# Kernel optimization log

Measured on AMD Instinct MI355X. Metric: run time of the kernel, lower is better.

Reference implementation:

```python
import jax, jax.numpy as jnp
import numpy as np

NUM_BITS_ACTS = 8
NUM_BITS_PARAMS = 8
NUM_BITS_ACCUM = 32


def quantized_range(num_bits):
    # distiller-style signed range: [-2^(n-1), 2^(n-1)-1]
    n = 2.0 ** num_bits
    return -n / 2.0, n / 2.0 - 1.0


def sym_scale(num_bits, sat_abs):
    # scale = (2^(n-1)-1) / max_abs
    return (2.0 ** (num_bits - 1) - 1.0) / sat_abs


def quant_clamp(t, scale, qmin, qmax):
    return jnp.clip(jnp.round(t * scale), qmin, qmax)


def setup_inputs() -> dict:
    key = jax.random.key(0)
    kx, kw = jax.random.split(key)
    x = jax.random.normal(kx, (8192, 4096), dtype=jnp.float32)
    W = jax.random.normal(kw, (4096, 4096), dtype=jnp.float32)  # [out, in]
    return {"x": x, "W": W}


def reference(x, W):
    acts_min, acts_max = quantized_range(NUM_BITS_ACTS)
    params_min, params_max = quantized_range(NUM_BITS_PARAMS)
    accum_min, accum_max = quantized_range(NUM_BITS_ACCUM)

    # __init__: quantize weights once (symmetric, max-abs)
    w_scale = sym_scale(NUM_BITS_PARAMS, jnp.max(jnp.abs(W)))
    W_q = quant_clamp(W, w_scale, params_min, params_max)

    # pre_quantized_forward: input scale from max-abs, quantize-clamp input
    in_scale = sym_scale(NUM_BITS_ACTS, jnp.max(jnp.abs(x)))
    x_q = quant_clamp(x, in_scale, acts_min, acts_max)

    # wrapped Linear in integer domain, clamp to accumulator range
    accum = jnp.clip(x_q @ W_q.T, accum_min, accum_max)  # [8192, 4096]

    # post_quantized_forward: requantize accumulator to output range
    accum_scale = in_scale * w_scale
    accum_max_abs = jnp.max(jnp.abs(accum))
    y_f_max_abs = accum_max_abs / accum_scale
    out_scale = sym_scale(NUM_BITS_ACTS, y_f_max_abs)
    requant_scale = out_scale / accum_scale

    out_q = quant_clamp(accum, requant_scale, acts_min, acts_max)
    out_f = out_q / out_scale  # dequantize
    return out_f
```

## Files before the change

### kernel.cpp

```cpp
#include <hip/hip_runtime.h>
#include <stdint.h>


using i32x4 = __attribute__((ext_vector_type(4))) int;

#define M_DIM 8192
#define N_DIM 4096
#define K_DIM 4096

#define BM 256
#define BN 256
#define BKB 128
#define NKT (K_DIM / BKB)

__global__ void k_init(unsigned* sc) {
    sc[0] = 0u;
    sc[1] = 0u;
    sc[2] = 0u;
}

__global__ __launch_bounds__(256) void k_absmax2(const float4* __restrict__ x,
                                                 const float4* __restrict__ w,
                                                 unsigned* __restrict__ sc) {
    const bool isX = blockIdx.x < 2048;
    const float4* src = isX ? x : w;
    const int n4 = isX ? (M_DIM * K_DIM / 4) : (N_DIM * K_DIM / 4);
    const int brel = isX ? blockIdx.x : (blockIdx.x - 2048);
    const int nb = isX ? 2048 : 1024;
    unsigned m = 0;
    for (int i = brel * 256 + threadIdx.x; i < n4; i += nb * 256) {
        float4 v = src[i];
        unsigned a = __float_as_uint(v.x) & 0x7fffffffu;
        unsigned b = __float_as_uint(v.y) & 0x7fffffffu;
        unsigned c = __float_as_uint(v.z) & 0x7fffffffu;
        unsigned d = __float_as_uint(v.w) & 0x7fffffffu;
        m = max(m, max(max(a, b), max(c, d)));
    }
    for (int off = 32; off; off >>= 1)
        m = max(m, (unsigned)__shfl_xor((int)m, off));
    __shared__ unsigned wm[4];
    int ln = threadIdx.x & 63, wv = threadIdx.x >> 6;
    if (ln == 0) wm[wv] = m;
    __syncthreads();
    if (threadIdx.x == 0)
        atomicMax(sc + (isX ? 0 : 1), max(max(wm[0], wm[1]), max(wm[2], wm[3])));
}

__global__ __launch_bounds__(256) void k_quant2(const float4* __restrict__ x,
                                                const float4* __restrict__ w,
                                                unsigned* __restrict__ xq,
                                                unsigned* __restrict__ wq,
                                                const unsigned* __restrict__ sc) {
    const bool isX = blockIdx.x < 2048;
    const float4* src = isX ? x : w;
    unsigned* dst = isX ? xq : wq;
    const int n4 = isX ? (M_DIM * K_DIM / 4) : (N_DIM * K_DIM / 4);
    const int brel = isX ? blockIdx.x : (blockIdx.x - 2048);
    const int nb = isX ? 2048 : 1024;
    const float scale = 127.0f / __uint_as_float(sc[isX ? 0 : 1]);
    for (int i = brel * 256 + threadIdx.x; i < n4; i += nb * 256) {
        float4 v = src[i];
        int q0 = min(127, max(-128, (int)rintf(v.x * scale)));
        int q1 = min(127, max(-128, (int)rintf(v.y * scale)));
        int q2 = min(127, max(-128, (int)rintf(v.z * scale)));
        int q3 = min(127, max(-128, (int)rintf(v.w * scale)));
        dst[i] = (unsigned)(q0 & 0xff) | ((unsigned)(q1 & 0xff) << 8) |
                 ((unsigned)(q2 & 0xff) << 16) | ((unsigned)(q3 & 0xff) << 24);
    }
}

__global__ __launch_bounds__(512, 2) void k_gemm(const char* __restrict__ Aq,
                                                 const char* __restrict__ Bq,
                                                 int* __restrict__ C,
                                                 unsigned* __restrict__ maxAcc) {
    __shared__ __align__(16) char lds[131072];
    __shared__ int wmax[8];

    const int t = threadIdx.x;
    const int ln = t & 63;
    const int wv = t >> 6;
    const int wr = wv >> 2;
    const int wc = wv & 3;
    const int lr = ln & 15;
    const int lk = ln >> 4;

    const int bid = blockIdx.x;
    const int swz = (bid & 7) * 64 + (bid >> 3);
    const int bx = swz & 15;
    const int by = swz >> 4;
    const int arow0 = by * BM;
    const int brow0 = bx * BN;

    const int cs0 = lk ^ (lr & 7);
    const int aoff0 = (((wr << 7) + lr) << 7) + (cs0 << 4);
    const int aoff1 = aoff0 ^ 64;
    const int boff0 = (((wc << 6) + lr) << 7) + (cs0 << 4);
    const int boff1 = boff0 ^ 64;

    int voffA[2], voffB[2];
#pragma unroll
    for (int it = 0; it < 2; ++it) {
        const int chunk = it * 512 + (wv << 6) + ln;
        const int row = chunk >> 3;
        const int gc = (chunk & 7) ^ (row & 7);
        voffA[it] = (arow0 + row) * 4096 + (gc << 4);
        voffB[it] = (brow0 + row) * 4096 + (gc << 4);
    }

    i32x4 acc[8][4];
#pragma unroll
    for (int i = 0; i < 8; ++i)
#pragma unroll
        for (int j = 0; j < 4; ++j) acc[i][j] = (i32x4)(0);

    auto STAGE = [&](int kt, int j) {
        const int slot = kt & 1;
        const int koff = kt * 128 + (j & 1) * 524288;
        const bool isA = (j < 2);
        const char* gbase = isA ? Aq : Bq;
        const int* voff = isA ? voffA : voffB;
        char* lbase = lds + (isA ? 0 : 65536) + (slot << 15) + ((j & 1) << 14) + (wv << 10);
#pragma unroll
        for (int it = 0; it < 2; ++it) {
            const char* g = gbase + (unsigned)(voff[it] + koff);
            __builtin_amdgcn_global_load_lds(
                (const __attribute__((address_space(1))) void*)g,
                (__attribute__((address_space(3))) void*)(lbase + (it << 13)), 16, 0, 0);
        }
    };

    STAGE(0, 0); STAGE(0, 1); STAGE(0, 2); STAGE(0, 3);
    STAGE(1, 2); STAGE(1, 3);
    asm volatile("s_waitcnt vmcnt(4)" ::: "memory");
    __builtin_amdgcn_s_barrier();
    __builtin_amdgcn_sched_barrier(0);

    for (int kt = 0; kt < NKT; ++kt) {
        const int sl = (kt & 1) << 15;
        const char* pA0 = lds + sl + aoff0;
        const char* pA1 = lds + sl + aoff1;
        const char* pB0 = lds + 65536 + sl + boff0;
        const char* pB1 = lds + 65536 + sl + boff1;
        i32x4 a[4][2], b[4][2];

#pragma unroll
        for (int mi = 0; mi < 4; ++mi) {
            a[mi][0] = *(const i32x4*)(pA0 + (mi << 11));
            a[mi][1] = *(const i32x4*)(pA1 + (mi << 11));
        }
#pragma unroll
        for (int ni = 0; ni < 4; ++ni) {
            b[ni][0] = *(const i32x4*)(pB0 + (ni << 11));
            b[ni][1] = *(const i32x4*)(pB1 + (ni << 11));
        }
        if (kt + 1 < NKT) { STAGE(kt + 1, 0); STAGE(kt + 1, 1); }
        __builtin_amdgcn_s_setprio(1);
#pragma unroll
        for (int kh = 0; kh < 2; ++kh)
#pragma unroll
            for (int mi = 0; mi < 4; ++mi)
#pragma unroll
                for (int ni = 0; ni < 4; ++ni)
                    acc[mi][ni] = __builtin_amdgcn_mfma_i32_16x16x64_i8(
                        a[mi][kh], b[ni][kh], acc[mi][ni], 0, 0, 0);
        __builtin_amdgcn_s_setprio(0);
        __builtin_amdgcn_s_barrier();
        __builtin_amdgcn_sched_barrier(0);

#pragma unroll
        for (int mi = 0; mi < 4; ++mi) {
            a[mi][0] = *(const i32x4*)(pA0 + ((mi + 4) << 11));
            a[mi][1] = *(const i32x4*)(pA1 + ((mi + 4) << 11));
        }
        if (kt + 2 < NKT) {
            STAGE(kt + 2, 2); STAGE(kt + 2, 3);
            asm volatile("s_waitcnt vmcnt(4)" ::: "memory");
        } else {
            asm volatile("s_waitcnt vmcnt(0)" ::: "memory");
        }
        __builtin_amdgcn_s_setprio(1);
#pragma unroll
        for (int kh = 0; kh < 2; ++kh)
#pragma unroll
            for (int mi = 0; mi < 4; ++mi)
#pragma unroll
                for (int ni = 0; ni < 4; ++ni)
                    acc[mi + 4][ni] = __builtin_amdgcn_mfma_i32_16x16x64_i8(
                        a[mi][kh], b[ni][kh], acc[mi + 4][ni], 0, 0, 0);
        __builtin_amdgcn_s_setprio(0);
        __builtin_amdgcn_s_barrier();
        __builtin_amdgcn_sched_barrier(0);
    }

    int amax = 0;
#pragma unroll
    for (int mi = 0; mi < 8; ++mi) {
#pragma unroll
        for (int ni = 0; ni < 4; ++ni) {
            const int row0 = arow0 + (wr << 7) + (mi << 4) + (lk << 2);
            const int col  = brow0 + (wc << 6) + (ni << 4) + lr;
            i32x4 v = acc[mi][ni];
#pragma unroll
            for (int j = 0; j < 4; ++j) {
                C[(size_t)(row0 + j) * N_DIM + col] = v[j];
                int a = v[j] < 0 ? -v[j] : v[j];
                amax = max(amax, a);
            }
        }
    }
    for (int off = 32; off; off >>= 1)
        amax = max(amax, __shfl_xor(amax, off));
    if (ln == 0) wmax[wv] = amax;
    __syncthreads();
    if (t == 0) {
        int m = wmax[0];
#pragma unroll
        for (int i = 1; i < 8; ++i) m = max(m, wmax[i]);
        atomicMax(maxAcc, (unsigned)m);
    }
}

__global__ __launch_bounds__(256) void k_requant(int4* __restrict__ buf, int n4,
                                                 const unsigned* __restrict__ sc) {
    const float maxX = __uint_as_float(sc[0]);
    const float maxW = __uint_as_float(sc[1]);
    const float maxA = (float)(int)sc[2];
    const float in_scale = 127.0f / maxX;
    const float w_scale  = 127.0f / maxW;
    const float accum_scale = in_scale * w_scale;
    const float requant = 127.0f / maxA;
    const float out_scale = requant * accum_scale;
    int stride = gridDim.x * blockDim.x;
    for (int i = blockIdx.x * blockDim.x + threadIdx.x; i < n4; i += stride) {
        int4 v = buf[i];
        float4 o;
        o.x = fminf(127.f, fmaxf(-128.f, rintf((float)v.x * requant))) / out_scale;
        o.y = fminf(127.f, fmaxf(-128.f, rintf((float)v.y * requant))) / out_scale;
        o.z = fminf(127.f, fmaxf(-128.f, rintf((float)v.z * requant))) / out_scale;
        o.w = fminf(127.f, fmaxf(-128.f, rintf((float)v.w * requant))) / out_scale;
        ((float4*)buf)[i] = o;
    }
}

extern "C" void kernel_launch(void* const* d_in, const int* in_sizes, int n_in,
                              void* d_out, int out_size, void* d_ws, size_t ws_size,
                              hipStream_t stream) {
    const float* x = (const float*)d_in[0];
    const float* W = (const float*)d_in[1];

    unsigned* sc = (unsigned*)d_ws;
    char* xq = (char*)d_ws + 256;
    char* wq = xq + (size_t)M_DIM * K_DIM;

    k_init<<<1, 1, 0, stream>>>(sc);
    k_absmax2<<<3072, 256, 0, stream>>>((const float4*)x, (const float4*)W, sc);
    k_quant2<<<3072, 256, 0, stream>>>((const float4*)x, (const float4*)W,
                                       (unsigned*)xq, (unsigned*)wq, sc);
    k_gemm<<<(M_DIM / BM) * (N_DIM / BN), 512, 0, stream>>>(xq, wq, (int*)d_out, sc + 2);
    k_requant<<<2048, 256, 0, stream>>>((int4*)d_out, M_DIM * N_DIM / 4, sc);
}
```

Baseline: 276.4 us.

## Fuse absmax and quantize into one persistent kernel with grid barrier

Merges the absmax reduction and quantization kernels into a single persistent kernel of 1024 blocks, which synchronize through an atomic counter grid barrier. Each block reduces its slice, waits for all blocks, reads the global max, then re-reads the same slice to quantize, so the second pass may partly hit cache and one launch is saved. It relies on all 1024 blocks being co-resident, or the spin barrier deadlocks. Each block's data slice (about 64 KB for x) is likely too large to stay in L2 between the passes.

```diff
diff --git a/kernel.cpp b/kernel.cpp
--- a/kernel.cpp
+++ b/kernel.cpp
@@ -13,20 +13,29 @@
 #define BKB 128
 #define NKT (K_DIM / BKB)
 
+#define NBQ 1024
+#define NBX 683
+
 __global__ void k_init(unsigned* sc) {
     sc[0] = 0u;
     sc[1] = 0u;
     sc[2] = 0u;
-}
-
-__global__ __launch_bounds__(256) void k_absmax2(const float4* __restrict__ x,
-                                                 const float4* __restrict__ w,
-                                                 unsigned* __restrict__ sc) {
-    const bool isX = blockIdx.x < 2048;
+    sc[3] = 0u;
+}
+
+__global__ __launch_bounds__(256) void k_quantfused(const float4* __restrict__ x,
+                                                    const float4* __restrict__ w,
+                                                    unsigned* __restrict__ xq,
+                                                    unsigned* __restrict__ wq,
+                                                    unsigned* __restrict__ sc) {
+    const bool isX = blockIdx.x < NBX;
     const float4* src = isX ? x : w;
+    unsigned* dst = isX ? xq : wq;
     const int n4 = isX ? (M_DIM * K_DIM / 4) : (N_DIM * K_DIM / 4);
-    const int brel = isX ? blockIdx.x : (blockIdx.x - 2048);
-    const int nb = isX ? 2048 : 1024;
+    const int brel = isX ? blockIdx.x : (blockIdx.x - NBX);
+    const int nb = isX ? NBX : (NBQ - NBX);
+    const int scIdx = isX ? 0 : 1;
+
     unsigned m = 0;
     for (int i = brel * 256 + threadIdx.x; i < n4; i += nb * 256) {
         float4 v = src[i];
@@ -39,25 +48,23 @@
     for (int off = 32; off; off >>= 1)
         m = max(m, (unsigned)__shfl_xor((int)m, off));
     __shared__ unsigned wm[4];
-    int ln = threadIdx.x & 63, wv = threadIdx.x >> 6;
+    __shared__ unsigned s_bits;
+    const int ln = threadIdx.x & 63, wv = threadIdx.x >> 6;
     if (ln == 0) wm[wv] = m;
     __syncthreads();
-    if (threadIdx.x == 0)
-        atomicMax(sc + (isX ? 0 : 1), max(max(wm[0], wm[1]), max(wm[2], wm[3])));
-}
-
-__global__ __launch_bounds__(256) void k_quant2(const float4* __restrict__ x,
-                                                const float4* __restrict__ w,
-                                                unsigned* __restrict__ xq,
-                                                unsigned* __restrict__ wq,
-                                                const unsigned* __restrict__ sc) {
-    const bool isX = blockIdx.x < 2048;
-    const float4* src = isX ? x : w;
-    unsigned* dst = isX ? xq : wq;
-    const int n4 = isX ? (M_DIM * K_DIM / 4) : (N_DIM * K_DIM / 4);
-    const int brel = isX ? blockIdx.x : (blockIdx.x - 2048);
-    const int nb = isX ? 2048 : 1024;
-    const float scale = 127.0f / __uint_as_float(sc[isX ? 0 : 1]);
+
+    if (threadIdx.x == 0) {
+        unsigned bm = max(max(wm[0], wm[1]), max(wm[2], wm[3]));
+        atomicMax(sc + scIdx, bm);
+        __threadfence();
+        atomicAdd(sc + 3, 1u);
+        while (atomicAdd(sc + 3, 0u) < NBQ)
+            __builtin_amdgcn_s_sleep(32);
+        s_bits = atomicAdd(sc + scIdx, 0u);
+    }
+    __syncthreads();
+
+    const float scale = 127.0f / __uint_as_float(s_bits);
     for (int i = brel * 256 + threadIdx.x; i < n4; i += nb * 256) {
         float4 v = src[i];
         int q0 = min(127, max(-128, (int)rintf(v.x * scale)));
@@ -253,9 +260,8 @@
     char* wq = xq + (size_t)M_DIM * K_DIM;
 
     k_init<<<1, 1, 0, stream>>>(sc);
-    k_absmax2<<<3072, 256, 0, stream>>>((const float4*)x, (const float4*)W, sc);
-    k_quant2<<<3072, 256, 0, stream>>>((const float4*)x, (const float4*)W,
-                                       (unsigned*)xq, (unsigned*)wq, sc);
+    k_quantfused<<<NBQ, 256, 0, stream>>>((const float4*)x, (const float4*)W,
+                                          (unsigned*)xq, (unsigned*)wq, sc);
     k_gemm<<<(M_DIM / BM) * (N_DIM / BN), 512, 0, stream>>>(xq, wq, (int*)d_out, sc + 2);
     k_requant<<<2048, 256, 0, stream>>>((int4*)d_out, M_DIM * N_DIM / 4, sc);
 }
```

After: 363.6 us. +31.6%, slower.

## Switch int8 GEMM from 16x16x64 to 32x32x32 MFMA tiles

Applied to the files above, without the earlier changes.

Replaces the 16x16x64 int8 MFMA with the 32x32x32 variant, reorganizing per-wave accumulators into 4x2 blocks of 16-wide vectors. It also rewrites the LDS fragment addressing (swizzled offsets per k-slice) and the epilogue's row/column mapping. Larger MFMA tiles raise arithmetic per LDS fragment load, cutting LDS read traffic and instruction count. In exchange the LDS access pattern changes, which may introduce bank conflicts, and the output store pattern changes.

```diff
diff --git a/kernel.cpp b/kernel.cpp
--- a/kernel.cpp
+++ b/kernel.cpp
@@ -2,7 +2,8 @@
 #include <stdint.h>
 
 
-using i32x4 = __attribute__((ext_vector_type(4))) int;
+using i32x4  = __attribute__((ext_vector_type(4))) int;
+using i32x16 = __attribute__((ext_vector_type(16))) int;
 
 #define M_DIM 8192
 #define N_DIM 4096
@@ -81,8 +82,9 @@
     const int wv = t >> 6;
     const int wr = wv >> 2;
     const int wc = wv & 3;
-    const int lr = ln & 15;
-    const int lk = ln >> 4;
+    const int l31 = ln & 31;
+    const int hi = ln >> 5;
+    const int r7 = ln & 7;
 
     const int bid = blockIdx.x;
     const int swz = (bid & 7) * 64 + (bid >> 3);
@@ -91,11 +93,14 @@
     const int arow0 = by * BM;
     const int brow0 = bx * BN;
 
-    const int cs0 = lk ^ (lr & 7);
-    const int aoff0 = (((wr << 7) + lr) << 7) + (cs0 << 4);
-    const int aoff1 = aoff0 ^ 64;
-    const int boff0 = (((wc << 6) + lr) << 7) + (cs0 << 4);
-    const int boff1 = boff0 ^ 64;
+    const int cs0 = r7 ^ hi;
+    int aoffk[4], boffk[4];
+#pragma unroll
+    for (int ks = 0; ks < 4; ++ks) {
+        const int off = (cs0 << 4) ^ (ks << 5);
+        aoffk[ks] = (((wr << 7) + l31) << 7) + off;
+        boffk[ks] = (((wc << 6) + l31) << 7) + off;
+    }
 
     int voffA[2], voffB[2];
 #pragma unroll
@@ -107,11 +112,11 @@
         voffB[it] = (brow0 + row) * 4096 + (gc << 4);
     }
 
-    i32x4 acc[8][4];
-#pragma unroll
-    for (int i = 0; i < 8; ++i)
-#pragma unroll
-        for (int j = 0; j < 4; ++j) acc[i][j] = (i32x4)(0);
+    i32x16 acc[4][2];
+#pragma unroll
+    for (int i = 0; i < 4; ++i)
+#pragma unroll
+        for (int j = 0; j < 2; ++j) acc[i][j] = (i32x16)(0);
 
     auto STAGE = [&](int kt, int j) {
         const int slot = kt & 1;
@@ -137,41 +142,39 @@
 
     for (int kt = 0; kt < NKT; ++kt) {
         const int sl = (kt & 1) << 15;
-        const char* pA0 = lds + sl + aoff0;
-        const char* pA1 = lds + sl + aoff1;
-        const char* pB0 = lds + 65536 + sl + boff0;
-        const char* pB1 = lds + 65536 + sl + boff1;
-        i32x4 a[4][2], b[4][2];
-
-#pragma unroll
-        for (int mi = 0; mi < 4; ++mi) {
-            a[mi][0] = *(const i32x4*)(pA0 + (mi << 11));
-            a[mi][1] = *(const i32x4*)(pA1 + (mi << 11));
-        }
-#pragma unroll
-        for (int ni = 0; ni < 4; ++ni) {
-            b[ni][0] = *(const i32x4*)(pB0 + (ni << 11));
-            b[ni][1] = *(const i32x4*)(pB1 + (ni << 11));
-        }
+        const char* lA_ = lds + sl;
+        const char* lB_ = lds + 65536 + sl;
+        i32x4 a[2][4], b[2][4];
+
+#pragma unroll
+        for (int mf = 0; mf < 2; ++mf)
+#pragma unroll
+            for (int ks = 0; ks < 4; ++ks)
+                a[mf][ks] = *(const i32x4*)(lA_ + aoffk[ks] + (mf << 12));
+#pragma unroll
+        for (int nf = 0; nf < 2; ++nf)
+#pragma unroll
+            for (int ks = 0; ks < 4; ++ks)
+                b[nf][ks] = *(const i32x4*)(lB_ + boffk[ks] + (nf << 12));
         if (kt + 1 < NKT) { STAGE(kt + 1, 0); STAGE(kt + 1, 1); }
         __builtin_amdgcn_s_setprio(1);
 #pragma unroll
-        for (int kh = 0; kh < 2; ++kh)
-#pragma unroll
-            for (int mi = 0; mi < 4; ++mi)
-#pragma unroll
-                for (int ni = 0; ni < 4; ++ni)
-                    acc[mi][ni] = __builtin_amdgcn_mfma_i32_16x16x64_i8(
-                        a[mi][kh], b[ni][kh], acc[mi][ni], 0, 0, 0);
+        for (int ks = 0; ks < 4; ++ks)
+#pragma unroll
+            for (int mf = 0; mf < 2; ++mf)
+#pragma unroll
+                for (int nf = 0; nf < 2; ++nf)
+                    acc[mf][nf] = __builtin_amdgcn_mfma_i32_32x32x32_i8(
+                        a[mf][ks], b[nf][ks], acc[mf][nf], 0, 0, 0);
         __builtin_amdgcn_s_setprio(0);
         __builtin_amdgcn_s_barrier();
         __builtin_amdgcn_sched_barrier(0);
 
 #pragma unroll
-        for (int mi = 0; mi < 4; ++mi) {
-            a[mi][0] = *(const i32x4*)(pA0 + ((mi + 4) << 11));
-            a[mi][1] = *(const i32x4*)(pA1 + ((mi + 4) << 11));
-        }
+        for (int mf = 0; mf < 2; ++mf)
+#pragma unroll
+            for (int ks = 0; ks < 4; ++ks)
+                a[mf][ks] = *(const i32x4*)(lA_ + aoffk[ks] + ((mf + 2) << 12));
         if (kt + 2 < NKT) {
             STAGE(kt + 2, 2); STAGE(kt + 2, 3);
             asm volatile("s_waitcnt vmcnt(4)" ::: "memory");
@@ -180,13 +183,13 @@
         }
         __builtin_amdgcn_s_setprio(1);
 #pragma unroll
-        for (int kh = 0; kh < 2; ++kh)
-#pragma unroll
-            for (int mi = 0; mi < 4; ++mi)
-#pragma unroll
-                for (int ni = 0; ni < 4; ++ni)
-                    acc[mi + 4][ni] = __builtin_amdgcn_mfma_i32_16x16x64_i8(
-                        a[mi][kh], b[ni][kh], acc[mi + 4][ni], 0, 0, 0);
+        for (int ks = 0; ks < 4; ++ks)
+#pragma unroll
+            for (int mf = 0; mf < 2; ++mf)
+#pragma unroll
+                for (int nf = 0; nf < 2; ++nf)
+                    acc[mf + 2][nf] = __builtin_amdgcn_mfma_i32_32x32x32_i8(
+                        a[mf][ks], b[nf][ks], acc[mf + 2][nf], 0, 0, 0);
         __builtin_amdgcn_s_setprio(0);
         __builtin_amdgcn_s_barrier();
         __builtin_amdgcn_sched_barrier(0);
@@ -194,16 +197,17 @@
 
     int amax = 0;
 #pragma unroll
-    for (int mi = 0; mi < 8; ++mi) {
-#pragma unroll
-        for (int ni = 0; ni < 4; ++ni) {
-            const int row0 = arow0 + (wr << 7) + (mi << 4) + (lk << 2);
-            const int col  = brow0 + (wc << 6) + (ni << 4) + lr;
-            i32x4 v = acc[mi][ni];
-#pragma unroll
-            for (int j = 0; j < 4; ++j) {
-                C[(size_t)(row0 + j) * N_DIM + col] = v[j];
-                int a = v[j] < 0 ? -v[j] : v[j];
+    for (int mf = 0; mf < 4; ++mf) {
+#pragma unroll
+        for (int nf = 0; nf < 2; ++nf) {
+            const int col = brow0 + (wc << 6) + (nf << 5) + l31;
+            const int rb  = arow0 + (wr << 7) + (mf << 5) + (hi << 2);
+            i32x16 v = acc[mf][nf];
+#pragma unroll
+            for (int reg = 0; reg < 16; ++reg) {
+                const int row = rb + (reg & 3) + ((reg >> 2) << 3);
+                C[(size_t)row * N_DIM + col] = v[reg];
+                int a = v[reg] < 0 ? -v[reg] : v[reg];
                 amax = max(amax, a);
             }
         }
```

Result: slower. 290.3 us (+5.0%).
